# Kernel tuning notes

Measured on AMD Instinct MI355X. Metric: run time of the kernel, lower is better.

The kernel has to match this reference:

```python
import jax, jax.numpy as jnp
import numpy as np
import math

# ----- module hyperparameters (init_kwargs) -----
TSTR_MIN = 0.1
TSTR_MAX = 100.0
N_TAUS = 50
K = 8
DT = 0.05
G = 1
DT_SCALE = 1.0
N = N_TAUS + 2 * K  # 66


def _build_consts():
    # log-spaced tau* grid with K pad nodes on each side
    c = (TSTR_MAX / TSTR_MIN) ** (1.0 / (N_TAUS - 1))
    exps = np.arange(-K, N_TAUS + K, dtype=np.float64)  # integers -k .. n_taus-1+k
    tau_stars_full = TSTR_MIN * c ** exps               # [N]
    s_full = K / tau_stars_full                          # [N]
    # first-derivative matrix in s (log-spaced stencil)
    D = np.zeros((N, N), dtype=np.float64)
    for i in range(1, N - 1):
        denom = s_full[i + 1] - s_full[i - 1]
        D[i, i - 1] = -(1.0 / c) / denom
        D[i, i] = (1.0 / c - c) / denom
        D[i, i + 1] = c / denom
    post_1 = ((-1.0) ** K) * np.linalg.matrix_power(D, K).T * tau_stars_full ** G
    log_post_2 = -math.lgamma(K + 1) + (K + 1) * np.log(s_full)
    post = post_1 * np.exp(log_post_2)                   # [N, N]
    return (jnp.asarray(s_full, dtype=jnp.float32),
            jnp.asarray(post, dtype=jnp.float32))

S_FULL, POST = _build_consts()


def setup_inputs() -> dict:
    key = jax.random.key(0)
    k1, _ = jax.random.split(key)
    T, B, F = 2048, 8, 64
    f = jax.random.uniform(k1, (T, B, F), dtype=jnp.float32) + 1e-3  # strictly positive input
    alpha = jnp.ones((T, B, F), dtype=jnp.float32)
    delta = jnp.zeros((T, B, F), dtype=jnp.float32)
    return {"f": f, "alpha": alpha, "delta": delta}


def reference(f, alpha, delta):
    T, B, F = f.shape
    # log Laplace decay per step: [T, B, F, N]
    log_lap = (alpha * DT + delta)[..., None] * (-S_FULL * DT_SCALE)
    # log of the input drive; nan -> 0 (torch nan_to_num), keep -inf for f == 0
    log_f = jnp.log(f * DT)
    log_f = jnp.nan_to_num(log_f, nan=0.0, posinf=jnp.inf, neginf=-jnp.inf)[..., None]  # [T,B,F,1]

    init = jnp.full((B, F, N), -jnp.inf, dtype=f.dtype)  # h = log(0)

    def step(carry, inp):
        ll, lf = inp
        new = jnp.logaddexp(carry + ll, lf)
        return new, new

    h, log_F_full = jax.lax.scan(step, init, (log_lap, jnp.broadcast_to(log_f, (T, B, F, 1))))
    # log_F_full: [T, B, F, N]
    F_exp = jnp.exp(log_F_full)
    til_f = jnp.einsum('tbfn,nm->tbfm', F_exp, POST)[..., K:-K]  # [T,B,F,n_taus]
    F_out = F_exp[..., K:-K]                                      # [T,B,F,n_taus]
    return til_f, h, F_out
```

## Files before the change

### kernel.cpp

```cpp
#include <hip/hip_runtime.h>
#include <math.h>

#define TDIM 2048
#define BF   512
#define NS   66
#define KK   8
#define DT   0.05f
#define MOUT 50
#define NC   16
#define LCH  128
#define STEP 64

#define WS_NS    0
#define WS_PB    128
#define WS_DBL   1024
#define WS_A     20480
#define WS_B     (WS_A + NC*BF*NS)
#define WS_CARRY (WS_B + NC*BF*NS)

#define OUT_TIL 0
#define OUT_H   (TDIM*BF*MOUT)
#define OUT_F   (OUT_H + BF*NS)

__device__ __forceinline__ double sv_d(double c, int i) {
    return 8.0 / (0.1 * pow(c, (double)(i - KK)));
}

__global__ void k_init(float* __restrict__ ws) {
    double* d1 = (double*)(ws + WS_DBL);
    double* d2 = d1 + NS * NS;
    const int tid = threadIdx.x;
    const double c = pow(1000.0, 1.0 / 49.0);

    for (int idx = tid; idx < NS * NS; idx += 512) d1[idx] = 0.0;
    __syncthreads();
    if (tid < NS - 2) {
        int i = tid + 1;
        double denom = sv_d(c, i + 1) - sv_d(c, i - 1);
        d1[i * NS + (i - 1)] = -(1.0 / c) / denom;
        d1[i * NS + i]       = (1.0 / c - c) / denom;
        d1[i * NS + (i + 1)] = c / denom;
    }
    __syncthreads();
    for (int r = 0; r < 3; r++) {
        double* src = (r & 1) ? d2 : d1;
        double* dst = (r & 1) ? d1 : d2;
        for (int idx = tid; idx < NS * NS; idx += 512) {
            int i = idx / NS, j = idx % NS;
            double acc = 0.0;
            for (int k = 0; k < NS; k++) acc += src[i * NS + k] * src[k * NS + j];
            dst[idx] = acc;
        }
        __syncthreads();
    }
    for (int idx = tid; idx < 17 * MOUT; idx += 512) {
        int k = idx / MOUT, j = idx % MOUT;
        int m = j + KK;
        int n = m - KK + k;
        double sm   = sv_d(c, m);
        double taum = 8.0 / sm;
        double post = d2[m * NS + n] * taum * pow(sm, 9.0) / 40320.0;
        ws[WS_PB + idx] = (float)post;
    }
    if (tid < NS) ws[WS_NS + tid] = (float)(-sv_d(c, tid));
}

__global__ __launch_bounds__(256, 8) void k_sum(const float* __restrict__ f,
                                                const float* __restrict__ alpha,
                                                const float* __restrict__ delta,
                                                float* __restrict__ ws) {
    __shared__ float2 xs[4][STEP];
    const int wid  = threadIdx.x >> 6;
    const int lane = threadIdx.x & 63;
    const int unit = blockIdx.x * 4 + wid;
    const int c  = unit >> 9;
    const int bf = unit & 511;

    const float nsv = ws[WS_NS + lane];
    const float ns2 = ws[WS_NS + 64 + (lane & 1)];

    const int t0 = c * LCH;
    const float* fp = f     + (size_t)t0 * BF + bf;
    const float* ap = alpha + (size_t)t0 * BF + bf;
    const float* dp = delta + (size_t)t0 * BF + bf;

    float A = 1.0f, Bc = 0.0f, A2 = 1.0f, B2 = 0.0f;
    for (int tb = 0; tb < LCH; tb += STEP) {
        float av = ap[(tb + lane) * BF];
        float dv = dp[(tb + lane) * BF];
        float fv = fp[(tb + lane) * BF];
        xs[wid][lane] = make_float2(fmaf(av, DT, dv), fv * DT);
#pragma unroll 8
        for (int tt = 0; tt < STEP; tt++) {
            float2 v = xs[wid][tt];
            float a = __expf(nsv * v.x);
            A *= a;  Bc = fmaf(Bc, a, v.y);
            float a2 = __expf(ns2 * v.x);
            A2 *= a2; B2 = fmaf(B2, a2, v.y);
        }
    }
    const int base = (c * BF + bf) * NS;
    ws[WS_A + base + lane] = A;
    ws[WS_B + base + lane] = Bc;
    if (lane < 2) {
        ws[WS_A + base + 64 + lane] = A2;
        ws[WS_B + base + 64 + lane] = B2;
    }
}

__global__ __launch_bounds__(256) void k_phase2(float* __restrict__ ws,
                                                float* __restrict__ out) {
    const int idx = blockIdx.x * 256 + threadIdx.x;
    const int bf = idx / NS;
    const int n  = idx - bf * NS;
    float F = 0.0f;
    for (int c = 0; c < NC; c++) {
        const int base = (c * BF + bf) * NS + n;
        ws[WS_CARRY + base] = F;
        F = fmaf(ws[WS_A + base], F, ws[WS_B + base]);
    }
    out[OUT_H + bf * NS + n] = logf(F);
}

__global__ __launch_bounds__(256) void k_phase3(const float* __restrict__ f,
                                                const float* __restrict__ alpha,
                                                const float* __restrict__ delta,
                                                const float* __restrict__ ws,
                                                float* __restrict__ out) {
    __shared__ float2 xs[4][STEP];
    const int wid  = threadIdx.x >> 6;
    const int lane = threadIdx.x & 63;
    const int unit = blockIdx.x * 4 + wid;
    const int c  = unit >> 9;
    const int bf = unit & 511;

    const float nsv  = ws[WS_NS + lane];
    const float ns64 = ws[WS_NS + 64];
    const float ns65 = ws[WS_NS + 65];
    const int j = lane - KK;
    const bool outl = (j >= 0) && (j < MOUT);
    const int ja = outl ? j : 0;

    float pm[17];
#pragma unroll
    for (int k = 0; k < 17; k++)
        pm[k] = outl ? ws[WS_PB + k * MOUT + j] : 0.0f;

    const int cb = (c * BF + bf) * NS;
    float F   = ws[WS_CARRY + cb + lane];
    float F64 = ws[WS_CARRY + cb + 64];
    float F65 = ws[WS_CARRY + cb + 65];

    const int t0 = c * LCH;
    const float* fp = f     + (size_t)t0 * BF + bf;
    const float* ap = alpha + (size_t)t0 * BF + bf;
    const float* dp = delta + (size_t)t0 * BF + bf;
    float* til = out + OUT_TIL + (size_t)t0 * BF * MOUT + bf * MOUT + ja;
    float* fo  = out + OUT_F   + (size_t)t0 * BF * MOUT + bf * MOUT + ja;

    for (int tb = 0; tb < LCH; tb += STEP) {
        float av = ap[(tb + lane) * BF];
        float dv = dp[(tb + lane) * BF];
        float fv = fp[(tb + lane) * BF];
        xs[wid][lane] = make_float2(fmaf(av, DT, dv), fv * DT);
#pragma unroll 4
        for (int tt = 0; tt < STEP; tt++) {
            float2 v = xs[wid][tt];

            float a = __expf(nsv * v.x);
            F = fmaf(F, a, v.y);
            float a64 = __expf(ns64 * v.x);
            F64 = fmaf(F64, a64, v.y);
            float a65 = __expf(ns65 * v.x);
            F65 = fmaf(F65, a65, v.y);

            float acc = pm[8] * F;
#pragma unroll
            for (int k = 0; k < 8; k++) {
                float vv = __shfl_up(F, 8 - k, 64);
                acc = fmaf(pm[k], vv, acc);
            }
#pragma unroll
            for (int k = 9; k < 17; k++) {
                float vv = __shfl_down(F, k - 8, 64);
                int idxn = lane - 8 + k;
                if (idxn == 64) vv = F64;
                else if (idxn == 65) vv = F65;
                acc = fmaf(pm[k], vv, acc);
            }

            if (outl) {
                til[0] = acc;
                fo[0]  = F;
            }
            til += BF * MOUT;
            fo  += BF * MOUT;
        }
    }
}

extern "C" void kernel_launch(void* const* d_in, const int* in_sizes, int n_in,
                              void* d_out, int out_size, void* d_ws, size_t ws_size,
                              hipStream_t stream) {
    const float* f     = (const float*)d_in[0];
    const float* alpha = (const float*)d_in[1];
    const float* delta = (const float*)d_in[2];
    float* out = (float*)d_out;
    float* ws  = (float*)d_ws;

    k_init  <<<1, 512, 0, stream>>>(ws);
    k_sum   <<<(BF * NC) / 4, 256, 0, stream>>>(f, alpha, delta, ws);
    k_phase2<<<(BF * NS) / 256, 256, 0, stream>>>(ws, out);
    k_phase3<<<(BF * NC) / 4, 256, 0, stream>>>(f, alpha, delta, ws, out);
}
```

Before: 805.9 us.

## Move init matmul to shared memory, use exp2 and cheaper phase3 extras

The setup kernel now does its double-precision matrix powers in shared memory instead of global workspace, with register-buffered accumulation, and precomputes s values. The decay rates are prescaled by log2(e) so the hot loops can use exp2f instead of __expf. In phase3, the two extra pad nodes are computed once per lane (lane parity) and broadcast with shuffles, replacing two extra exponentials per step for every lane. The output stores use 32-bit offsets, and the unroll and occupancy hints are raised. The trade-off is two more shuffles per step and more register pressure from the deeper unroll.

```diff
diff --git a/kernel.cpp b/kernel.cpp
--- a/kernel.cpp
+++ b/kernel.cpp
@@ -4,6 +4,7 @@
 #define TDIM 2048
 #define BF   512
 #define NS   66
+#define NS2  (NS*NS)
 #define KK   8
 #define DT   0.05f
 #define MOUT 50
@@ -13,7 +14,6 @@
 
 #define WS_NS    0
 #define WS_PB    128
-#define WS_DBL   1024
 #define WS_A     20480
 #define WS_B     (WS_A + NC*BF*NS)
 #define WS_CARRY (WS_B + NC*BF*NS)
@@ -22,47 +22,54 @@
 #define OUT_H   (TDIM*BF*MOUT)
 #define OUT_F   (OUT_H + BF*NS)
 
-__device__ __forceinline__ double sv_d(double c, int i) {
-    return 8.0 / (0.1 * pow(c, (double)(i - KK)));
-}
-
-__global__ void k_init(float* __restrict__ ws) {
-    double* d1 = (double*)(ws + WS_DBL);
-    double* d2 = d1 + NS * NS;
+__global__ __launch_bounds__(512) void k_init(float* __restrict__ ws) {
+    __shared__ double sd[NS2];
+    __shared__ double sv[NS];
     const int tid = threadIdx.x;
     const double c = pow(1000.0, 1.0 / 49.0);
 
-    for (int idx = tid; idx < NS * NS; idx += 512) d1[idx] = 0.0;
+    if (tid < NS) sv[tid] = 8.0 / (0.1 * pow(c, (double)(tid - KK)));
+    for (int idx = tid; idx < NS2; idx += 512) sd[idx] = 0.0;
     __syncthreads();
-    if (tid < NS - 2) {
-        int i = tid + 1;
-        double denom = sv_d(c, i + 1) - sv_d(c, i - 1);
-        d1[i * NS + (i - 1)] = -(1.0 / c) / denom;
-        d1[i * NS + i]       = (1.0 / c - c) / denom;
-        d1[i * NS + (i + 1)] = c / denom;
+    if (tid >= 1 && tid < NS - 1) {
+        const int i = tid;
+        double denom = sv[i + 1] - sv[i - 1];
+        sd[i * NS + (i - 1)] = -(1.0 / c) / denom;
+        sd[i * NS + i]       = (1.0 / c - c) / denom;
+        sd[i * NS + (i + 1)] = c / denom;
     }
     __syncthreads();
     for (int r = 0; r < 3; r++) {
-        double* src = (r & 1) ? d2 : d1;
-        double* dst = (r & 1) ? d1 : d2;
-        for (int idx = tid; idx < NS * NS; idx += 512) {
-            int i = idx / NS, j = idx % NS;
-            double acc = 0.0;
-            for (int k = 0; k < NS; k++) acc += src[i * NS + k] * src[k * NS + j];
-            dst[idx] = acc;
+        double acc[9];
+#pragma unroll
+        for (int u = 0; u < 9; u++) {
+            const int idx = tid + u * 512;
+            double a = 0.0;
+            if (idx < NS2) {
+                const int i = idx / NS, j = idx - i * NS;
+                const double* Ri = sd + i * NS;
+#pragma unroll 6
+                for (int k = 0; k < NS; k++) a += Ri[k] * sd[k * NS + j];
+            }
+            acc[u] = a;
         }
         __syncthreads();
+#pragma unroll
+        for (int u = 0; u < 9; u++) {
+            const int idx = tid + u * 512;
+            if (idx < NS2) sd[idx] = acc[u];
+        }
+        __syncthreads();
     }
     for (int idx = tid; idx < 17 * MOUT; idx += 512) {
-        int k = idx / MOUT, j = idx % MOUT;
-        int m = j + KK;
-        int n = m - KK + k;
-        double sm   = sv_d(c, m);
-        double taum = 8.0 / sm;
-        double post = d2[m * NS + n] * taum * pow(sm, 9.0) / 40320.0;
+        const int k = idx / MOUT, j = idx - k * MOUT;
+        const int m = j + KK;
+        const int n = m - KK + k;
+        const double smv = sv[m];
+        double post = sd[m * NS + n] * (8.0 / smv) * pow(smv, 9.0) / 40320.0;
         ws[WS_PB + idx] = (float)post;
     }
-    if (tid < NS) ws[WS_NS + tid] = (float)(-sv_d(c, tid));
+    if (tid < NS) ws[WS_NS + tid] = (float)(-sv[tid] * 1.4426950408889634);
 }
 
 __global__ __launch_bounds__(256, 8) void k_sum(const float* __restrict__ f,
@@ -93,9 +100,9 @@
 #pragma unroll 8
         for (int tt = 0; tt < STEP; tt++) {
             float2 v = xs[wid][tt];
-            float a = __expf(nsv * v.x);
+            float a = exp2f(nsv * v.x);
             A *= a;  Bc = fmaf(Bc, a, v.y);
-            float a2 = __expf(ns2 * v.x);
+            float a2 = exp2f(ns2 * v.x);
             A2 *= a2; B2 = fmaf(B2, a2, v.y);
         }
     }
@@ -122,11 +129,11 @@
     out[OUT_H + bf * NS + n] = logf(F);
 }
 
-__global__ __launch_bounds__(256) void k_phase3(const float* __restrict__ f,
-                                                const float* __restrict__ alpha,
-                                                const float* __restrict__ delta,
-                                                const float* __restrict__ ws,
-                                                float* __restrict__ out) {
+__global__ __launch_bounds__(256, 8) void k_phase3(const float* __restrict__ f,
+                                                   const float* __restrict__ alpha,
+                                                   const float* __restrict__ delta,
+                                                   const float* __restrict__ ws,
+                                                   float* __restrict__ out) {
     __shared__ float2 xs[4][STEP];
     const int wid  = threadIdx.x >> 6;
     const int lane = threadIdx.x & 63;
@@ -134,9 +141,8 @@
     const int c  = unit >> 9;
     const int bf = unit & 511;
 
-    const float nsv  = ws[WS_NS + lane];
-    const float ns64 = ws[WS_NS + 64];
-    const float ns65 = ws[WS_NS + 65];
+    const float nsv = ws[WS_NS + lane];
+    const float ns2 = ws[WS_NS + 64 + (lane & 1)];
     const int j = lane - KK;
     const bool outl = (j >= 0) && (j < MOUT);
     const int ja = outl ? j : 0;
@@ -147,32 +153,32 @@
         pm[k] = outl ? ws[WS_PB + k * MOUT + j] : 0.0f;
 
     const int cb = (c * BF + bf) * NS;
-    float F   = ws[WS_CARRY + cb + lane];
-    float F64 = ws[WS_CARRY + cb + 64];
-    float F65 = ws[WS_CARRY + cb + 65];
+    float F  = ws[WS_CARRY + cb + lane];
+    float F2 = ws[WS_CARRY + cb + 64 + (lane & 1)];
 
     const int t0 = c * LCH;
     const float* fp = f     + (size_t)t0 * BF + bf;
     const float* ap = alpha + (size_t)t0 * BF + bf;
     const float* dp = delta + (size_t)t0 * BF + bf;
-    float* til = out + OUT_TIL + (size_t)t0 * BF * MOUT + bf * MOUT + ja;
-    float* fo  = out + OUT_F   + (size_t)t0 * BF * MOUT + bf * MOUT + ja;
+    unsigned off_til = (unsigned)(OUT_TIL + t0 * BF * MOUT + bf * MOUT + ja);
+    unsigned off_fo  = (unsigned)(OUT_F   + t0 * BF * MOUT + bf * MOUT + ja);
 
     for (int tb = 0; tb < LCH; tb += STEP) {
         float av = ap[(tb + lane) * BF];
         float dv = dp[(tb + lane) * BF];
         float fv = fp[(tb + lane) * BF];
         xs[wid][lane] = make_float2(fmaf(av, DT, dv), fv * DT);
-#pragma unroll 4
+#pragma unroll 8
         for (int tt = 0; tt < STEP; tt++) {
             float2 v = xs[wid][tt];
 
-            float a = __expf(nsv * v.x);
+            float a = exp2f(nsv * v.x);
             F = fmaf(F, a, v.y);
-            float a64 = __expf(ns64 * v.x);
-            F64 = fmaf(F64, a64, v.y);
-            float a65 = __expf(ns65 * v.x);
-            F65 = fmaf(F65, a65, v.y);
+            float a2 = exp2f(ns2 * v.x);
+            F2 = fmaf(F2, a2, v.y);
+
+            float f64 = __shfl(F2, 0, 64);
+            float f65 = __shfl(F2, 1, 64);
 
             float acc = pm[8] * F;
 #pragma unroll
@@ -184,17 +190,17 @@
             for (int k = 9; k < 17; k++) {
                 float vv = __shfl_down(F, k - 8, 64);
                 int idxn = lane - 8 + k;
-                if (idxn == 64) vv = F64;
-                else if (idxn == 65) vv = F65;
+                if (idxn == 64) vv = f64;
+                else if (idxn == 65) vv = f65;
                 acc = fmaf(pm[k], vv, acc);
             }
 
             if (outl) {
-                til[0] = acc;
-                fo[0]  = F;
-            }
-            til += BF * MOUT;
-            fo  += BF * MOUT;
+                out[off_til] = acc;
+                out[off_fo]  = F;
+            }
+            off_til += BF * MOUT;
+            off_fo  += BF * MOUT;
         }
     }
 }
```

New measurement: 726.2 us. -9.9%, faster.
